# Kernel optimization log

Measured on AMD Instinct MI355X. Metric: run time of the kernel, lower is better.

Reference implementation:

```python
import jax, jax.numpy as jnp
import numpy as np

B, IN, H = 8192, 512, 512


def _binarize(w):
    # sign() forward with straight-through gradient (ebnn Binarize)
    return w + jax.lax.stop_gradient(jnp.sign(w) - w)


def setup_inputs() -> dict:
    key = jax.random.key(0)
    ks = jax.random.split(key, 7)
    stdv = 1.0 / np.sqrt(H)
    return {
        "x": jax.random.normal(ks[0], (B, IN), jnp.float32),
        "hx": jax.random.normal(ks[1], (B, H), jnp.float32),
        "cx": jax.random.normal(ks[2], (B, H), jnp.float32),
        "W_ih": jax.random.uniform(ks[3], (4 * H, IN), jnp.float32, -stdv, stdv),
        "W_hh": jax.random.uniform(ks[4], (4 * H, H), jnp.float32, -stdv, stdv),
        "bias_ih": jax.random.uniform(ks[5], (4 * H,), jnp.float32, -stdv, stdv),
        "bias_hh": jax.random.uniform(ks[6], (4 * H,), jnp.float32, -stdv, stdv),
    }


def reference(x, hx, cx, W_ih, W_hh, bias_ih, bias_hh):
    # gates: [B, 4H] = x @ sign(W_ih)^T + b_ih + hx @ sign(W_hh)^T + b_hh
    gates = (jnp.einsum("bi,gi->bg", x, _binarize(W_ih)) + bias_ih
             + jnp.einsum("bh,gh->bg", hx, _binarize(W_hh)) + bias_hh)
    ingate, forgetgate, cellgate, outgate = jnp.split(gates, 4, axis=1)
    cy = jax.nn.sigmoid(forgetgate) * cx + jax.nn.sigmoid(ingate) * jnp.tanh(cellgate)
    hy = jax.nn.sigmoid(outgate) * jnp.tanh(cy)
    return (hy, cy)
```

## Files before the change

kernel.cpp:

```cpp
#include <hip/hip_runtime.h>
#include <hip/hip_bf16.h>
#include <stdint.h>


typedef __attribute__((ext_vector_type(4))) int int4x;
typedef __attribute__((ext_vector_type(4))) float float4x;

#define B_DIM 8192
#define H_DIM 512

__device__ __forceinline__ float bf2f(uint16_t u) {
  return __uint_as_float(((uint32_t)u) << 16);
}
__device__ __forceinline__ uint16_t f2bf(float f) {
  uint32_t u = __float_as_uint(f);
  return (uint16_t)((u + 0x7FFFu + ((u >> 16) & 1u)) >> 16);
}
__device__ __forceinline__ float sigm(float x) { return 1.0f / (1.0f + __expf(-x)); }
__device__ __forceinline__ float tanh_f(float x) { return 2.0f / (1.0f + __expf(-2.0f * x)) - 1.0f; }

__device__ __forceinline__ int detect_f32(const void* x) {
  const int l = threadIdx.x & 63;
  uint32_t wrd = ((const uint32_t*)x)[l];
  uint32_t e0 = (wrd >> 7) & 0xFFu, e1 = (wrd >> 23) & 0xFFu;
  return __ballot(e0 > 0x85u || e1 > 0x85u) != 0ull;
}

__device__ __forceinline__ void quant4(const float* v, uint32_t* hi4, uint32_t* lo4) {
  uint32_t h = 0, lo = 0;
#pragma unroll
  for (int j = 0; j < 4; ++j) {
    float c = fminf(fmaxf(v[j], -8.0f), 8.0f);
    int xf = __float2int_rn(c * 4096.0f);
    xf = xf > 32639 ? 32639 : xf;
    xf = xf < -32768 ? -32768 : xf;
    const int lb = (xf << 24) >> 24;
    const int hb = (xf - lb) >> 8;
    lo |= ((uint32_t)lb & 0xFFu) << (8 * j);
    h |= ((uint32_t)hb & 0xFFu) << (8 * j);
  }
  *hi4 = h;
  *lo4 = lo;
}

__device__ __forceinline__ void gload16(const void* g, void* l) {
  __builtin_amdgcn_global_load_lds(
      (const __attribute__((address_space(1))) unsigned int*)g,
      (__attribute__((address_space(3))) unsigned int*)l, 16, 0, 0);
}

__global__ __launch_bounds__(256) void prep_kernel(
    const void* __restrict__ x, const void* __restrict__ hx,
    const void* __restrict__ w_ih, const void* __restrict__ w_hh,
    int8_t* __restrict__ Xhi, int8_t* __restrict__ Xlo, int8_t* __restrict__ Bp) {
  __shared__ alignas(16) char lsc[33280];
  const int isF32 = detect_f32(x);
  const int t = threadIdx.x;
  const int w = t >> 6, l = t & 63;
  const int isX = blockIdx.x < 512;
  const int grp = isX ? blockIdx.x : (blockIdx.x - 512);

#pragma unroll
  for (int rr = 0; rr < 4; ++rr) {
    const int r = w * 4 + rr;
    long rowbase;
    if (isX) rowbase = (long)(grp * 16 + r) * 512;
    else     rowbase = (long)((grp & 3) * 512 + (grp >> 2) * 16 + r) * 512;
#pragma unroll
    for (int src = 0; src < 2; ++src) {
      const void* sp_ = isX ? (src ? hx : x) : (src ? w_hh : w_ih);
      const int k = src * 512 + l * 8;
      float v[8];
      if (isF32) {
        const float* fp = (const float*)sp_ + rowbase + l * 8;
        float4x f0 = *(const float4x*)fp;
        float4x f1 = *(const float4x*)(fp + 4);
#pragma unroll
        for (int j = 0; j < 4; ++j) { v[j] = f0[j]; v[4 + j] = f1[j]; }
      } else {
        int4x raw = *(const int4x*)((const uint16_t*)sp_ + rowbase + l * 8);
        const uint16_t* u = (const uint16_t*)&raw;
#pragma unroll
        for (int j = 0; j < 8; ++j) v[j] = bf2f(u[j]);
      }
      if (isX) {
        uint32_t h0, lo0, h1, lo1;
        quant4(v, &h0, &lo0);
        quant4(v + 4, &h1, &lo1);
        *(uint32_t*)(lsc + r * 1040 + k) = h0;
        *(uint32_t*)(lsc + r * 1040 + k + 4) = h1;
        *(uint32_t*)(lsc + 16640 + r * 1040 + k) = lo0;
        *(uint32_t*)(lsc + 16640 + r * 1040 + k + 4) = lo1;
      } else {
        uint32_t s0 = 0, s1 = 0;
#pragma unroll
        for (int j = 0; j < 4; ++j) {
          const int a = v[j] > 0.f ? 1 : (v[j] < 0.f ? -1 : 0);
          const int b = v[4 + j] > 0.f ? 1 : (v[4 + j] < 0.f ? -1 : 0);
          s0 |= ((uint32_t)a & 0xFFu) << (8 * j);
          s1 |= ((uint32_t)b & 0xFFu) << (8 * j);
        }
        *(uint32_t*)(lsc + r * 1040 + k) = s0;
        *(uint32_t*)(lsc + r * 1040 + k + 4) = s1;
      }
    }
  }
  __syncthreads();
  const int kt = t >> 4, quad = (t >> 2) & 3, rb = (t & 3) * 4;
  const int loff = kt * 64 + quad * 16;
  if (isX) {
    int4x h[4], lo[4];
#pragma unroll
    for (int i = 0; i < 4; ++i) {
      h[i] = *(const int4x*)(lsc + (rb + i) * 1040 + loff);
      lo[i] = *(const int4x*)(lsc + 16640 + (rb + i) * 1040 + loff);
    }
    int4x* dh = (int4x*)(Xhi + (long)grp * 16384 + t * 64);
    int4x* dl = (int4x*)(Xlo + (long)grp * 16384 + t * 64);
#pragma unroll
    for (int i = 0; i < 4; ++i) { dh[i] = h[i]; dl[i] = lo[i]; }
  } else {
    int4x s[4];
#pragma unroll
    for (int i = 0; i < 4; ++i)
      s[i] = *(const int4x*)(lsc + (rb + i) * 1040 + loff);
    int4x* db = (int4x*)(Bp + (long)grp * 16384 + t * 64);
#pragma unroll
    for (int i = 0; i < 4; ++i) db[i] = s[i];
  }
}

__global__ __launch_bounds__(512) void blstm_gemm_kernel(
    const int8_t* __restrict__ Xhi, const int8_t* __restrict__ Xlo,
    const int8_t* __restrict__ Bp, const void* __restrict__ b_ih,
    const void* __restrict__ b_hh, const void* __restrict__ cx,
    const void* __restrict__ xdet, void* __restrict__ out) {
  __shared__ alignas(16) char lds[73728];
  const int tid = threadIdx.x;
  const int l = tid & 63, w = tid >> 6;
  const int lrow = l & 15, lq = l >> 4;
  const int wy = w >> 1, wx = w & 1;
  const int isF32 = detect_f32(xdet);
  const int bid = blockIdx.x;
  const int by = (bid & 7) * 8 + ((bid >> 3) & 7);
  const int bx = bid >> 6;

  const int8_t* csrc[3];
  int cdst[3];
#pragma unroll
  for (int i = 0; i < 3; ++i) {
    const int c = w * 3 + i;
    if (c < 8) {
      csrc[i] = Xhi + (((long)(by * 8 + c)) << 14) + l * 16;
      cdst[i] = c * 1024;
    } else if (c < 16) {
      csrc[i] = Xlo + (((long)(by * 8 + (c - 8))) << 14) + l * 16;
      cdst[i] = 8192 + (c - 8) * 1024;
    } else {
      csrc[i] = Bp + (((long)(bx * 8 + (c - 16))) << 14) + l * 16;
      cdst[i] = 16384 + (c - 16) * 1024;
    }
  }

  int4x acch[2][4], accl[2][4];
#pragma unroll
  for (int mt = 0; mt < 2; ++mt)
#pragma unroll
    for (int g = 0; g < 4; ++g) {
      acch[mt][g] = (int4x){0, 0, 0, 0};
      accl[mt][g] = (int4x){0, 0, 0, 0};
    }

#pragma unroll
  for (int i = 0; i < 3; ++i) gload16(csrc[i], lds + cdst[i]);
#pragma unroll
  for (int i = 0; i < 3; ++i) gload16(csrc[i] + 1024, lds + 24576 + cdst[i]);
  asm volatile("s_waitcnt vmcnt(3)\n\ts_barrier" ::: "memory");

#pragma unroll
  for (int ks = 0; ks < 16; ++ks) {
    const int cb = (ks % 3) * 24576;
    if (ks < 14) {
      const int nb = ((ks + 2) % 3) * 24576;
#pragma unroll
      for (int i = 0; i < 3; ++i)
        gload16(csrc[i] + (long)(ks + 2) * 1024, lds + nb + cdst[i]);
    }
    int4x ah[2], al[2], b[4];
#pragma unroll
    for (int mt = 0; mt < 2; ++mt) {
      ah[mt] = *(const int4x*)(lds + cb + (wy * 2 + mt) * 1024 + l * 16);
      al[mt] = *(const int4x*)(lds + cb + 8192 + (wy * 2 + mt) * 1024 + l * 16);
    }
#pragma unroll
    for (int g = 0; g < 4; ++g)
      b[g] = *(const int4x*)(lds + cb + 16384 + (wx * 4 + g) * 1024 + l * 16);
    __builtin_amdgcn_s_setprio(1);
#pragma unroll
    for (int mt = 0; mt < 2; ++mt)
#pragma unroll
      for (int g = 0; g < 4; ++g) {
        acch[mt][g] = __builtin_amdgcn_mfma_i32_16x16x64_i8(ah[mt], b[g], acch[mt][g], 0, 0, 0);
        accl[mt][g] = __builtin_amdgcn_mfma_i32_16x16x64_i8(al[mt], b[g], accl[mt][g], 0, 0, 0);
      }
    __builtin_amdgcn_s_setprio(0);
    if (ks < 14)
      asm volatile("s_waitcnt vmcnt(3)\n\ts_waitcnt lgkmcnt(0)\n\ts_barrier" ::: "memory");
    else if (ks == 14)
      asm volatile("s_waitcnt vmcnt(0)\n\ts_waitcnt lgkmcnt(0)\n\ts_barrier" ::: "memory");
  }

  const long CYo = (long)B_DIM * H_DIM;
  const int c = bx * 32 + wx * 16 + lrow;
  float biasv[4];
#pragma unroll
  for (int g = 0; g < 4; ++g) {
    if (isF32)
      biasv[g] = ((const float*)b_ih)[g * 512 + c] + ((const float*)b_hh)[g * 512 + c];
    else
      biasv[g] = bf2f(((const uint16_t*)b_ih)[g * 512 + c]) + bf2f(((const uint16_t*)b_hh)[g * 512 + c]);
  }
  float* outF = (float*)out;
  uint16_t* outB = (uint16_t*)out;
#pragma unroll
  for (int mt = 0; mt < 2; ++mt) {
#pragma unroll
    for (int r = 0; r < 4; ++r) {
      const int row = by * 128 + wy * 32 + mt * 16 + lq * 4 + r;
      const long cidx = (long)row * H_DIM + c;
      float vg[4];
#pragma unroll
      for (int g = 0; g < 4; ++g)
        vg[g] = fmaf((float)acch[mt][g][r], 0.0625f,
                     fmaf((float)accl[mt][g][r], 2.44140625e-4f, biasv[g]));
      const float cxv = isF32 ? ((const float*)cx)[cidx] : bf2f(((const uint16_t*)cx)[cidx]);
      const float ig = sigm(vg[0]), fg = sigm(vg[1]), og = sigm(vg[3]);
      const float cg = tanh_f(vg[2]);
      const float cy = fg * cxv + ig * cg;
      const float hy = og * tanh_f(cy);
      if (isF32) {
        outF[cidx] = hy;
        outF[CYo + cidx] = cy;
      } else {
        outB[cidx] = f2bf(hy);
        outB[CYo + cidx] = f2bf(cy);
      }
    }
  }
}

extern "C" void kernel_launch(void* const* d_in, const int* in_sizes, int n_in,
                              void* d_out, int out_size, void* d_ws, size_t ws_size,
                              hipStream_t stream) {
  const void* x = d_in[0];
  const void* hx = d_in[1];
  const void* cx = d_in[2];
  const void* W_ih = d_in[3];
  const void* W_hh = d_in[4];
  const void* b_ih = d_in[5];
  const void* b_hh = d_in[6];
  char* ws = (char*)d_ws;
  int8_t* Xhi = (int8_t*)ws;
  int8_t* Xlo = (int8_t*)(ws + 8388608);
  int8_t* Bp = (int8_t*)(ws + 16777216);

  prep_kernel<<<640, 256, 0, stream>>>(x, hx, W_ih, W_hh, Xhi, Xlo, Bp);
  blstm_gemm_kernel<<<1024, 512, 0, stream>>>(Xhi, Xlo, Bp, b_ih, b_hh, cx, x, d_out);
}
```

Baseline: 154.0 us.

## Switch int8 GEMM to 32x32x32 MFMA with matching 32-row packed layout

Replaces the 16x16x64 int8 MFMA tiles with 32x32x32 MFMA, and repacks the quantized activations and sign weights in the prep kernel into 32-row tiles so each LDS fragment feeds the larger instruction. The prep kernel now handles 32 rows per block with half as many blocks. The epilogue uses cross-lane shuffles to collect the four gates for each output element from the new accumulator layout. The goal is fewer MFMA issues and fewer LDS fragment reads per K step. The cost is shuffle overhead and half the lanes sitting idle in the epilogue.

```diff
diff --git a/kernel.cpp b/kernel.cpp
--- a/kernel.cpp
+++ b/kernel.cpp
@@ -4,6 +4,7 @@
 
 
 typedef __attribute__((ext_vector_type(4))) int int4x;
+typedef __attribute__((ext_vector_type(16))) int int16x;
 typedef __attribute__((ext_vector_type(4))) float float4x;
 
 #define B_DIM 8192
@@ -53,19 +54,22 @@
     const void* __restrict__ x, const void* __restrict__ hx,
     const void* __restrict__ w_ih, const void* __restrict__ w_hh,
     int8_t* __restrict__ Xhi, int8_t* __restrict__ Xlo, int8_t* __restrict__ Bp) {
-  __shared__ alignas(16) char lsc[33280];
+  __shared__ alignas(16) char lsc[66560];
   const int isF32 = detect_f32(x);
   const int t = threadIdx.x;
   const int w = t >> 6, l = t & 63;
-  const int isX = blockIdx.x < 512;
-  const int grp = isX ? blockIdx.x : (blockIdx.x - 512);
-
-#pragma unroll
-  for (int rr = 0; rr < 4; ++rr) {
-    const int r = w * 4 + rr;
+  const int isX = blockIdx.x < 256;
+  const int grp = isX ? blockIdx.x : (blockIdx.x - 256);
+
+#pragma unroll
+  for (int rr = 0; rr < 8; ++rr) {
+    const int r = w * 8 + rr;
     long rowbase;
-    if (isX) rowbase = (long)(grp * 16 + r) * 512;
-    else     rowbase = (long)((grp & 3) * 512 + (grp >> 2) * 16 + r) * 512;
+    if (isX) rowbase = (long)(grp * 32 + r) * 512;
+    else {
+      const int gp = grp & 1, hs = grp >> 1;
+      rowbase = (long)((gp * 2 + (r >> 4)) * 512 + hs * 16 + (r & 15)) * 512;
+    }
 #pragma unroll
     for (int src = 0; src < 2; ++src) {
       const void* sp_ = isX ? (src ? hx : x) : (src ? w_hh : w_ih);
@@ -89,8 +93,8 @@
         quant4(v + 4, &h1, &lo1);
         *(uint32_t*)(lsc + r * 1040 + k) = h0;
         *(uint32_t*)(lsc + r * 1040 + k + 4) = h1;
-        *(uint32_t*)(lsc + 16640 + r * 1040 + k) = lo0;
-        *(uint32_t*)(lsc + 16640 + r * 1040 + k + 4) = lo1;
+        *(uint32_t*)(lsc + 33280 + r * 1040 + k) = lo0;
+        *(uint32_t*)(lsc + 33280 + r * 1040 + k + 4) = lo1;
       } else {
         uint32_t s0 = 0, s1 = 0;
 #pragma unroll
@@ -106,27 +110,28 @@
     }
   }
   __syncthreads();
-  const int kt = t >> 4, quad = (t >> 2) & 3, rb = (t & 3) * 4;
-  const int loff = kt * 64 + quad * 16;
+  const int u = t & 7;
+  const int koff = (t >> 4) * 64 + ((t >> 3) & 1) * 32 + (u >> 2) * 16;
+  const int rbase = (u & 3) * 8;
   if (isX) {
-    int4x h[4], lo[4];
-#pragma unroll
-    for (int i = 0; i < 4; ++i) {
-      h[i] = *(const int4x*)(lsc + (rb + i) * 1040 + loff);
-      lo[i] = *(const int4x*)(lsc + 16640 + (rb + i) * 1040 + loff);
-    }
-    int4x* dh = (int4x*)(Xhi + (long)grp * 16384 + t * 64);
-    int4x* dl = (int4x*)(Xlo + (long)grp * 16384 + t * 64);
-#pragma unroll
-    for (int i = 0; i < 4; ++i) { dh[i] = h[i]; dl[i] = lo[i]; }
+    int4x h[8], lo[8];
+#pragma unroll
+    for (int i = 0; i < 8; ++i) {
+      h[i] = *(const int4x*)(lsc + (rbase + i) * 1040 + koff);
+      lo[i] = *(const int4x*)(lsc + 33280 + (rbase + i) * 1040 + koff);
+    }
+    int4x* dh = (int4x*)(Xhi + (long)grp * 32768 + t * 128);
+    int4x* dl = (int4x*)(Xlo + (long)grp * 32768 + t * 128);
+#pragma unroll
+    for (int i = 0; i < 8; ++i) { dh[i] = h[i]; dl[i] = lo[i]; }
   } else {
-    int4x s[4];
-#pragma unroll
-    for (int i = 0; i < 4; ++i)
-      s[i] = *(const int4x*)(lsc + (rb + i) * 1040 + loff);
-    int4x* db = (int4x*)(Bp + (long)grp * 16384 + t * 64);
-#pragma unroll
-    for (int i = 0; i < 4; ++i) db[i] = s[i];
+    int4x s[8];
+#pragma unroll
+    for (int i = 0; i < 8; ++i)
+      s[i] = *(const int4x*)(lsc + (rbase + i) * 1040 + koff);
+    int4x* db = (int4x*)(Bp + (long)grp * 32768 + t * 128);
+#pragma unroll
+    for (int i = 0; i < 8; ++i) db[i] = s[i];
   }
 }
 
@@ -138,7 +143,6 @@
   __shared__ alignas(16) char lds[73728];
   const int tid = threadIdx.x;
   const int l = tid & 63, w = tid >> 6;
-  const int lrow = l & 15, lq = l >> 4;
   const int wy = w >> 1, wx = w & 1;
   const int isF32 = detect_f32(xdet);
   const int bid = blockIdx.x;
@@ -151,30 +155,30 @@
   for (int i = 0; i < 3; ++i) {
     const int c = w * 3 + i;
     if (c < 8) {
-      csrc[i] = Xhi + (((long)(by * 8 + c)) << 14) + l * 16;
+      csrc[i] = Xhi + (((long)(by * 4 + (c >> 1))) << 15) + (c & 1) * 1024 + l * 16;
       cdst[i] = c * 1024;
     } else if (c < 16) {
-      csrc[i] = Xlo + (((long)(by * 8 + (c - 8))) << 14) + l * 16;
-      cdst[i] = 8192 + (c - 8) * 1024;
+      const int cA = c - 8;
+      csrc[i] = Xlo + (((long)(by * 4 + (cA >> 1))) << 15) + (cA & 1) * 1024 + l * 16;
+      cdst[i] = 8192 + cA * 1024;
     } else {
-      csrc[i] = Bp + (((long)(bx * 8 + (c - 16))) << 14) + l * 16;
-      cdst[i] = 16384 + (c - 16) * 1024;
-    }
-  }
-
-  int4x acch[2][4], accl[2][4];
-#pragma unroll
-  for (int mt = 0; mt < 2; ++mt)
-#pragma unroll
-    for (int g = 0; g < 4; ++g) {
-      acch[mt][g] = (int4x){0, 0, 0, 0};
-      accl[mt][g] = (int4x){0, 0, 0, 0};
-    }
+      const int cB = c - 16;
+      csrc[i] = Bp + (((long)(bx * 4 + (cB >> 1))) << 15) + (cB & 1) * 1024 + l * 16;
+      cdst[i] = 16384 + cB * 1024;
+    }
+  }
+
+  int16x acch[2], accl[2];
+#pragma unroll
+  for (int cc = 0; cc < 2; ++cc) {
+#pragma unroll
+    for (int r = 0; r < 16; ++r) { acch[cc][r] = 0; accl[cc][r] = 0; }
+  }
 
 #pragma unroll
   for (int i = 0; i < 3; ++i) gload16(csrc[i], lds + cdst[i]);
 #pragma unroll
-  for (int i = 0; i < 3; ++i) gload16(csrc[i] + 1024, lds + 24576 + cdst[i]);
+  for (int i = 0; i < 3; ++i) gload16(csrc[i] + 2048, lds + 24576 + cdst[i]);
   asm volatile("s_waitcnt vmcnt(3)\n\ts_barrier" ::: "memory");
 
 #pragma unroll
@@ -184,24 +188,26 @@
       const int nb = ((ks + 2) % 3) * 24576;
 #pragma unroll
       for (int i = 0; i < 3; ++i)
-        gload16(csrc[i] + (long)(ks + 2) * 1024, lds + nb + cdst[i]);
-    }
-    int4x ah[2], al[2], b[4];
-#pragma unroll
-    for (int mt = 0; mt < 2; ++mt) {
-      ah[mt] = *(const int4x*)(lds + cb + (wy * 2 + mt) * 1024 + l * 16);
-      al[mt] = *(const int4x*)(lds + cb + 8192 + (wy * 2 + mt) * 1024 + l * 16);
-    }
-#pragma unroll
-    for (int g = 0; g < 4; ++g)
-      b[g] = *(const int4x*)(lds + cb + 16384 + (wx * 4 + g) * 1024 + l * 16);
+        gload16(csrc[i] + (long)(ks + 2) * 2048, lds + nb + cdst[i]);
+    }
+    int4x ah[2], al[2], bb[2][2];
+#pragma unroll
+    for (int s = 0; s < 2; ++s) {
+      ah[s] = *(const int4x*)(lds + cb + (wy * 2 + s) * 1024 + l * 16);
+      al[s] = *(const int4x*)(lds + cb + 8192 + (wy * 2 + s) * 1024 + l * 16);
+    }
+#pragma unroll
+    for (int cc = 0; cc < 2; ++cc)
+#pragma unroll
+      for (int s = 0; s < 2; ++s)
+        bb[cc][s] = *(const int4x*)(lds + cb + 16384 + ((wx * 2 + cc) * 2 + s) * 1024 + l * 16);
     __builtin_amdgcn_s_setprio(1);
 #pragma unroll
-    for (int mt = 0; mt < 2; ++mt)
-#pragma unroll
-      for (int g = 0; g < 4; ++g) {
-        acch[mt][g] = __builtin_amdgcn_mfma_i32_16x16x64_i8(ah[mt], b[g], acch[mt][g], 0, 0, 0);
-        accl[mt][g] = __builtin_amdgcn_mfma_i32_16x16x64_i8(al[mt], b[g], accl[mt][g], 0, 0, 0);
+    for (int s = 0; s < 2; ++s)
+#pragma unroll
+      for (int cc = 0; cc < 2; ++cc) {
+        acch[cc] = __builtin_amdgcn_mfma_i32_32x32x32_i8(ah[s], bb[cc][s], acch[cc], 0, 0, 0);
+        accl[cc] = __builtin_amdgcn_mfma_i32_32x32x32_i8(al[s], bb[cc][s], accl[cc], 0, 0, 0);
       }
     __builtin_amdgcn_s_setprio(0);
     if (ks < 14)
@@ -211,31 +217,35 @@
   }
 
   const long CYo = (long)B_DIM * H_DIM;
-  const int c = bx * 32 + wx * 16 + lrow;
+  const int b = (l >> 4) & 1;
+  const int hcol = bx * 32 + wx * 16 + (l & 15);
   float biasv[4];
 #pragma unroll
   for (int g = 0; g < 4; ++g) {
     if (isF32)
-      biasv[g] = ((const float*)b_ih)[g * 512 + c] + ((const float*)b_hh)[g * 512 + c];
+      biasv[g] = ((const float*)b_ih)[g * 512 + hcol] + ((const float*)b_hh)[g * 512 + hcol];
     else
-      biasv[g] = bf2f(((const uint16_t*)b_ih)[g * 512 + c]) + bf2f(((const uint16_t*)b_hh)[g * 512 + c]);
+      biasv[g] = bf2f(((const uint16_t*)b_ih)[g * 512 + hcol]) + bf2f(((const uint16_t*)b_hh)[g * 512 + hcol]);
   }
   float* outF = (float*)out;
   uint16_t* outB = (uint16_t*)out;
-#pragma unroll
-  for (int mt = 0; mt < 2; ++mt) {
-#pragma unroll
-    for (int r = 0; r < 4; ++r) {
-      const int row = by * 128 + wy * 32 + mt * 16 + lq * 4 + r;
-      const long cidx = (long)row * H_DIM + c;
-      float vg[4];
-#pragma unroll
-      for (int g = 0; g < 4; ++g)
-        vg[g] = fmaf((float)acch[mt][g][r], 0.0625f,
-                     fmaf((float)accl[mt][g][r], 2.44140625e-4f, biasv[g]));
+  const int rowb = by * 128 + wy * 32 + 4 * (l >> 5);
+#pragma unroll
+  for (int r = 0; r < 16; ++r) {
+    const float raw0 = fmaf((float)acch[0][r], 0.0625f, (float)accl[0][r] * 2.44140625e-4f);
+    const float raw1 = fmaf((float)acch[1][r], 0.0625f, (float)accl[1][r] * 2.44140625e-4f);
+    const float o0 = __shfl_xor(raw0, 16);
+    const float o1 = __shfl_xor(raw1, 16);
+    const float g0 = (b ? o0 : raw0) + biasv[0];
+    const float g1 = (b ? raw0 : o0) + biasv[1];
+    const float g2 = (b ? o1 : raw1) + biasv[2];
+    const float g3 = (b ? raw1 : o1) + biasv[3];
+    if (b ? (r >= 8) : (r < 8)) {
+      const int row = rowb + (r & 3) + 8 * (r >> 2);
+      const long cidx = (long)row * H_DIM + hcol;
       const float cxv = isF32 ? ((const float*)cx)[cidx] : bf2f(((const uint16_t*)cx)[cidx]);
-      const float ig = sigm(vg[0]), fg = sigm(vg[1]), og = sigm(vg[3]);
-      const float cg = tanh_f(vg[2]);
+      const float ig = sigm(g0), fg = sigm(g1), og = sigm(g3);
+      const float cg = tanh_f(g2);
       const float cy = fg * cxv + ig * cg;
       const float hy = og * tanh_f(cy);
       if (isF32) {
@@ -264,6 +274,6 @@
   int8_t* Xlo = (int8_t*)(ws + 8388608);
   int8_t* Bp = (int8_t*)(ws + 16777216);
 
-  prep_kernel<<<640, 256, 0, stream>>>(x, hx, W_ih, W_hh, Xhi, Xlo, Bp);
+  prep_kernel<<<320, 256, 0, stream>>>(x, hx, W_ih, W_hh, Xhi, Xlo, Bp);
   blstm_gemm_kernel<<<1024, 512, 0, stream>>>(Xhi, Xlo, Bp, b_ih, b_hh, cx, x, d_out);
 }
```

Result: slower. 170.6 us (+10.8%).
